# Optimization experiments

Hardware: AMD Instinct MI355X
Metric: run time of the kernel (lower is better)

## Reference

```python
import jax, jax.numpy as jnp
import numpy as np

MAXLEN = 20
NLAYERS = 4


def setup_inputs() -> dict:
    key = jax.random.key(0)
    ks = jax.random.split(key, 16)
    B, SRC, H, V = 256, 64, 1024, 32000
    s = 1.0 / np.sqrt(H)
    return {
        "encoder_outputs": jax.random.normal(ks[0], (B, SRC, H), jnp.float32),
        "encoder_hidden": jax.random.normal(ks[1], (NLAYERS, B, H), jnp.float32),
        "emb_table": jax.random.normal(ks[2], (V, H), jnp.float32) * s,
        "gru_w_ih": jax.random.normal(ks[3], (NLAYERS, 3 * H, H), jnp.float32) * s,
        "gru_w_hh": jax.random.normal(ks[4], (NLAYERS, 3 * H, H), jnp.float32) * s,
        "gru_b_ih": jax.random.normal(ks[5], (NLAYERS, 3 * H), jnp.float32) * s,
        "gru_b_hh": jax.random.normal(ks[6], (NLAYERS, 3 * H), jnp.float32) * s,
        "out_w": jax.random.normal(ks[7], (V, H), jnp.float32) * s,
        "out_b": jax.random.normal(ks[8], (V,), jnp.float32) * s,
        "l1_w": jax.random.normal(ks[9], (3, 2 * H), jnp.float32) * s,
        "l1_b": jax.random.normal(ks[10], (3,), jnp.float32) * s,
        "l2_w": jax.random.normal(ks[11], (1, 3), jnp.float32),
        "l2_b": jax.random.normal(ks[12], (1,), jnp.float32),
    }


def _gru_layer(x, h, w_ih, w_hh, b_ih, b_hh):
    # PyTorch GRU gate order: r, z, n
    gi = x @ w_ih.T + b_ih  # [B, 3H]
    gh = h @ w_hh.T + b_hh  # [B, 3H]
    i_r, i_z, i_n = jnp.split(gi, 3, axis=-1)
    h_r, h_z, h_n = jnp.split(gh, 3, axis=-1)
    r = jax.nn.sigmoid(i_r + h_r)
    z = jax.nn.sigmoid(i_z + h_z)
    n = jnp.tanh(i_n + r * h_n)
    return (1.0 - z) * n + z * h


def reference(encoder_outputs, encoder_hidden, emb_table, gru_w_ih, gru_w_hh,
              gru_b_ih, gru_b_hh, out_w, out_b, l1_w, l1_b, l2_w, l2_b):
    B = encoder_outputs.shape[0]
    enc_h0 = encoder_hidden[0]  # [B, H]

    def step(carry, _):
        h, tok = carry  # h: [4,B,H], tok: [B] int32
        # attention-score branch (computed in torch but unused -> DCE'd by jit)
        a = jnp.broadcast_to(h[0, -1], enc_h0.shape)
        enc = jnp.concatenate([a, enc_h0], axis=1)  # [B, 2H]
        _align = jax.nn.softmax((enc @ l1_w.T + l1_b) @ l2_w.T + l2_b, axis=0)
        # embedding + relu + 4-layer GRU (seq len 1)
        x = jax.nn.relu(emb_table[tok])  # [B, H]
        hs = []
        for l in range(NLAYERS):
            hl = _gru_layer(x, h[l], gru_w_ih[l], gru_w_hh[l], gru_b_ih[l], gru_b_hh[l])
            hs.append(hl)
            x = hl
        h = jnp.stack(hs)  # [4, B, H]
        logits = x @ out_w.T + out_b  # [B, V]
        tok = jnp.argmax(logits, axis=-1).astype(jnp.int32)  # greedy (topk(1))
        return (h, tok), logits

    tok0 = jnp.zeros((B,), jnp.int32)
    (h_final, _), logits = jax.lax.scan(step, (encoder_hidden, tok0), None, length=MAXLEN)
    # [T,B,V] -> [B,T,V], then log_softmax over vocab
    log_probs = jax.nn.log_softmax(jnp.transpose(logits, (1, 0, 2)), axis=-1)
    return log_probs, h_final
```

## Files before the change

### kernel.cpp

```cpp
#include <hip/hip_runtime.h>
#include <math.h>

#define HD 1024
#define NBATCH 256
#define VOC 32000
#define TSTEPS 20
#define OUT_ROW 640000LL
#define BH ((size_t)NBATCH * HD)
#define NCHUNK 500
#define THR 0.125f

typedef _Float16 f16;
typedef __attribute__((ext_vector_type(4))) _Float16 f16x4;
typedef __attribute__((ext_vector_type(8))) _Float16 f16x8;
typedef __attribute__((ext_vector_type(4))) float f32x4;

#define GLOBAL_AS __attribute__((address_space(1)))
#define LDS_AS    __attribute__((address_space(3)))

static __device__ __forceinline__ float sigmoidf_(float v) {
  return 1.0f / (1.0f + expf(-v));
}


__global__ void f32_to_f16_k(const float* __restrict__ in, f16* __restrict__ out, long n8) {
  long i = (long)blockIdx.x * 256 + threadIdx.x;
  long stride = (long)gridDim.x * 256;
  for (; i < n8; i += stride) {
    float4 a = *((const float4*)in + i * 2);
    float4 b = *((const float4*)in + i * 2 + 1);
    f16x8 o;
    o[0] = (f16)a.x; o[1] = (f16)a.y; o[2] = (f16)a.z; o[3] = (f16)a.w;
    o[4] = (f16)b.x; o[5] = (f16)b.y; o[6] = (f16)b.z; o[7] = (f16)b.w;
    *((f16x8*)out + i) = o;
  }
}

__global__ void split_f32_k(const float* __restrict__ in, f16* __restrict__ hi,
                            f16* __restrict__ lo, long n8) {
  long i = (long)blockIdx.x * 256 + threadIdx.x;
  long stride = (long)gridDim.x * 256;
  for (; i < n8; i += stride) {
    float4 a = *((const float4*)in + i * 2);
    float4 b = *((const float4*)in + i * 2 + 1);
    float v[8] = {a.x, a.y, a.z, a.w, b.x, b.y, b.z, b.w};
    f16x8 h8, l8;
    #pragma unroll
    for (int j = 0; j < 8; ++j) {
      f16 h = (f16)v[j];
      h8[j] = h;
      l8[j] = (f16)(v[j] - (float)h);
    }
    *((f16x8*)hi + i) = h8;
    *((f16x8*)lo + i) = l8;
  }
}

__global__ __launch_bounds__(256)
void gemm_gru_mfma4_k(const f16* __restrict__ a0_hi, const f16* __restrict__ a0_lo,
                      const f16* __restrict__ a1_hi, const f16* __restrict__ a1_lo,
                      const float* __restrict__ emb, const int* __restrict__ tok, int use_emb,
                      const float* __restrict__ w_ih, const float* __restrict__ w_hh,
                      float* __restrict__ gg2) {
  __shared__ f16x8 atoms[2][1088];

  const int tid = threadIdx.x;
  const int lane = tid & 63;
  const int wave = tid >> 6;
  const int wm = wave >> 1, wn = wave & 1;
  const int l15 = lane & 15, l4 = lane >> 4;
  const int n0g = blockIdx.x * 64;
  const int m0 = blockIdx.y * 64;
  const int kb = blockIdx.z * 512;

  const f16 *ahi, *alo; const float* W; int nc;
  if (n0g < 3072) { ahi = a0_hi; alo = a0_lo; W = w_ih; nc = n0g; }
  else            { ahi = a1_hi; alo = a1_lo; W = w_hh; nc = n0g - 3072; }
  const bool embmode = use_emb && (n0g < 3072);

  f32x4 acc[2][2];
  #pragma unroll
  for (int mi = 0; mi < 2; ++mi)
    #pragma unroll
    for (int ni = 0; ni < 2; ++ni) acc[mi][ni] = (f32x4){0.f, 0.f, 0.f, 0.f};

  const int sr = tid >> 2, skg = tid & 3;
  const int satom = skg * 68 + sr;
  const float* wgp = W + (size_t)(nc + sr) * HD + kb + skg * 8;
  const f16* agh = ahi + (size_t)(m0 + sr) * HD + kb + skg * 8;
  const f16* agl = alo + (size_t)(m0 + sr) * HD + kb + skg * 8;
  const float* egp = embmode ? (emb + (size_t)tok[m0 + sr] * HD + kb + skg * 8) : wgp;

  #define LOADREGS(k0, rah, ral, wbh, wbl) { \
    if (embmode) { \
      float4 e0 = *(const float4*)(egp + (k0)); \
      float4 e1 = *(const float4*)(egp + (k0) + 4); \
      float av[8] = {fmaxf(e0.x,0.f), fmaxf(e0.y,0.f), fmaxf(e0.z,0.f), fmaxf(e0.w,0.f), \
                     fmaxf(e1.x,0.f), fmaxf(e1.y,0.f), fmaxf(e1.z,0.f), fmaxf(e1.w,0.f)}; \
      _Pragma("unroll") \
      for (int j = 0; j < 8; ++j) { \
        f16 h = (f16)av[j]; rah[j] = h; ral[j] = (f16)(av[j] - (float)h); \
      } \
    } else { \
      rah = *(const f16x8*)(agh + (k0)); \
      ral = *(const f16x8*)(agl + (k0)); \
    } \
    float4 w0 = *(const float4*)(wgp + (k0)); \
    float4 w1 = *(const float4*)(wgp + (k0) + 4); \
    float wv[8] = {w0.x, w0.y, w0.z, w0.w, w1.x, w1.y, w1.z, w1.w}; \
    _Pragma("unroll") \
    for (int j = 0; j < 8; ++j) { \
      f16 h = (f16)wv[j]; wbh[j] = h; wbl[j] = (f16)(wv[j] - (float)h); \
    } }

  {
    f16x8 rah, ral, wbh, wbl;
    LOADREGS(0, rah, ral, wbh, wbl);
    atoms[0][satom]       = rah;
    atoms[0][272 + satom] = ral;
    atoms[0][544 + satom] = wbh;
    atoms[0][816 + satom] = wbl;
  }
  __syncthreads();

  for (int kt = 0; kt < 16; ++kt) {
    const int cur = kt & 1;
    f16x8 nah, nal, nbh, nbl;
    if (kt < 15) { LOADREGS((kt + 1) * 32, nah, nal, nbh, nbl); }

    f16x8 fah[2], fal[2], fbh[2], fbl[2];
    #pragma unroll
    for (int mi = 0; mi < 2; ++mi) {
      int idx = l4 * 68 + wm * 32 + mi * 16 + l15;
      fah[mi] = atoms[cur][idx];
      fal[mi] = atoms[cur][272 + idx];
    }
    #pragma unroll
    for (int ni = 0; ni < 2; ++ni) {
      int idx = l4 * 68 + wn * 32 + ni * 16 + l15;
      fbh[ni] = atoms[cur][544 + idx];
      fbl[ni] = atoms[cur][816 + idx];
    }
    #pragma unroll
    for (int mi = 0; mi < 2; ++mi)
      #pragma unroll
      for (int ni = 0; ni < 2; ++ni) {
        acc[mi][ni] = __builtin_amdgcn_mfma_f32_16x16x32_f16(fah[mi], fbh[ni], acc[mi][ni], 0, 0, 0);
        acc[mi][ni] = __builtin_amdgcn_mfma_f32_16x16x32_f16(fah[mi], fbl[ni], acc[mi][ni], 0, 0, 0);
        acc[mi][ni] = __builtin_amdgcn_mfma_f32_16x16x32_f16(fal[mi], fbh[ni], acc[mi][ni], 0, 0, 0);
      }

    if (kt < 15) {
      atoms[cur ^ 1][satom]       = nah;
      atoms[cur ^ 1][272 + satom] = nal;
      atoms[cur ^ 1][544 + satom] = nbh;
      atoms[cur ^ 1][816 + satom] = nbl;
    }
    __syncthreads();
  }
  #undef LOADREGS

  float* outp = gg2 + (size_t)blockIdx.z * NBATCH * 6144;
  #pragma unroll
  for (int mi = 0; mi < 2; ++mi)
    #pragma unroll
    for (int ni = 0; ni < 2; ++ni) {
      const int col = n0g + wn * 32 + ni * 16 + l15;
      #pragma unroll
      for (int r = 0; r < 4; ++r) {
        const int row = m0 + wm * 32 + mi * 16 + l4 * 4 + r;
        outp[(size_t)row * 6144 + col] = acc[mi][ni][r];
      }
    }
}

static __device__ __forceinline__ float4 add4_(float4 a, float4 b) {
  float4 r; r.x = a.x + b.x; r.y = a.y + b.y; r.z = a.z + b.z; r.w = a.w + b.w; return r;
}
__global__ void gru_gates_split2_k(const float* __restrict__ gg2,
                                   const float* __restrict__ b_ih, const float* __restrict__ b_hh,
                                   const f16* __restrict__ hold_hi, const f16* __restrict__ hold_lo,
                                   f16* __restrict__ hnew_hi, f16* __restrict__ hnew_lo) {
  int idx = blockIdx.x * 256 + threadIdx.x;
  int b = idx >> 8;
  int k4 = (idx & 255) << 2;
  const float* g0 = gg2 + (size_t)b * 6144;
  const float* g1 = gg2 + (size_t)NBATCH * 6144 + (size_t)b * 6144;
  #define LD2(off) add4_(*(const float4*)(g0 + (off) + k4), *(const float4*)(g1 + (off) + k4))
  float4 gir = LD2(0);
  float4 giz = LD2(1024);
  float4 gin = LD2(2048);
  float4 ghr = LD2(3072);
  float4 ghz = LD2(4096);
  float4 ghn = LD2(5120);
  #undef LD2
  float4 bir = *(const float4*)(b_ih + k4);
  float4 biz = *(const float4*)(b_ih + 1024 + k4);
  float4 bin = *(const float4*)(b_ih + 2048 + k4);
  float4 bhr = *(const float4*)(b_hh + k4);
  float4 bhz = *(const float4*)(b_hh + 1024 + k4);
  float4 bhn = *(const float4*)(b_hh + 2048 + k4);
  f16x4 hh = *(const f16x4*)(hold_hi + (size_t)b * HD + k4);
  f16x4 hl = *(const f16x4*)(hold_lo + (size_t)b * HD + k4);
  float hov[4];
  #pragma unroll
  for (int j = 0; j < 4; ++j) hov[j] = (float)hh[j] + (float)hl[j];
  float4 ho; ho.x = hov[0]; ho.y = hov[1]; ho.z = hov[2]; ho.w = hov[3];
  float4 o;
  #define GATE(c) { \
    float rr = sigmoidf_(gir.c + bir.c + ghr.c + bhr.c); \
    float zz = sigmoidf_(giz.c + biz.c + ghz.c + bhz.c); \
    float nn = tanhf(gin.c + bin.c + rr * (ghn.c + bhn.c)); \
    o.c = (1.0f - zz) * nn + zz * ho.c; }
  GATE(x) GATE(y) GATE(z) GATE(w)
  #undef GATE
  float vv[4] = {o.x, o.y, o.z, o.w};
  f16x4 h4, l4;
  #pragma unroll
  for (int j = 0; j < 4; ++j) {
    f16 h = (f16)vv[j];
    h4[j] = h;
    l4[j] = (f16)(vv[j] - (float)h);
  }
  *(f16x4*)(hnew_hi + (size_t)b * HD + k4) = h4;
  *(f16x4*)(hnew_lo + (size_t)b * HD + k4) = l4;
}

__global__ __launch_bounds__(256)
void gemm_logits3_k(const f16* __restrict__ xf, const f16* __restrict__ wf,
                    const float* __restrict__ bias, float* __restrict__ scr,
                    float* __restrict__ pmax, float* __restrict__ psum) {
  __shared__ f16 lb[2][2112];
  const int tid = threadIdx.x;
  const int lane = tid & 63;
  const int wave = tid >> 6;
  const int l15 = lane & 15, l4 = lane >> 4;
  const int chunk = blockIdx.x;
  const int n0 = chunk * 64;

  f32x4 acc[4][4];
  #pragma unroll
  for (int mi = 0; mi < 4; ++mi)
    #pragma unroll
    for (int ni = 0; ni < 4; ++ni) acc[mi][ni] = (f32x4){0.f, 0.f, 0.f, 0.f};

  f16x8 a_cur[4], a_nxt[4];

  #define STAGE(k0, buf) { \
    const f16* src = wf + (size_t)(n0 + lane) * 1024 + (k0) + wave * 8; \
    __builtin_amdgcn_global_load_lds((const GLOBAL_AS void*)src, \
        (LDS_AS void*)(lb[buf] + wave * 528), 16, 0, 0); }
  #define LOADA(k0, dst) { \
    _Pragma("unroll") \
    for (int mi = 0; mi < 4; ++mi) { \
      int row = wave * 64 + mi * 16 + l15; \
      dst[mi] = *(const f16x8*)(xf + (size_t)row * 1024 + (k0) + l4 * 8); \
    } }

  STAGE(0, 0);
  LOADA(0, a_cur);
  __syncthreads();

  for (int kt = 0; kt < 32; ++kt) {
    const int cur = kt & 1;
    f16x8 b[4];
    #pragma unroll
    for (int ni = 0; ni < 4; ++ni)
      b[ni] = *(const f16x8*)(lb[cur] + (size_t)l4 * 528 + (size_t)(ni * 16 + l15) * 8);
    if (kt < 31) {
      STAGE((kt + 1) * 32, cur ^ 1);
      LOADA((kt + 1) * 32, a_nxt);
    }
    #pragma unroll
    for (int mi = 0; mi < 4; ++mi)
      #pragma unroll
      for (int ni = 0; ni < 4; ++ni)
        acc[mi][ni] = __builtin_amdgcn_mfma_f32_16x16x32_f16(a_cur[mi], b[ni], acc[mi][ni], 0, 0, 0);
    __syncthreads();
    #pragma unroll
    for (int mi = 0; mi < 4; ++mi) a_cur[mi] = a_nxt[mi];
  }
  #undef STAGE
  #undef LOADA

  float bv[4];
  #pragma unroll
  for (int ni = 0; ni < 4; ++ni) bv[ni] = bias[n0 + ni * 16 + l15];

  #pragma unroll
  for (int mi = 0; mi < 4; ++mi) {
    #pragma unroll
    for (int r = 0; r < 4; ++r) {
      const int row = wave * 64 + mi * 16 + l4 * 4 + r;
      float v[4];
      #pragma unroll
      for (int ni = 0; ni < 4; ++ni) {
        v[ni] = acc[mi][ni][r] + bv[ni];
        scr[(size_t)row * VOC + n0 + ni * 16 + l15] = v[ni];
      }
      float m = fmaxf(fmaxf(v[0], v[1]), fmaxf(v[2], v[3]));
      #pragma unroll
      for (int d = 1; d < 16; d <<= 1) m = fmaxf(m, __shfl_xor(m, d, 64));
      float s = __expf(v[0] - m) + __expf(v[1] - m) + __expf(v[2] - m) + __expf(v[3] - m);
      #pragma unroll
      for (int d = 1; d < 16; d <<= 1) s += __shfl_xor(s, d, 64);
      if (l15 == 0) {
        pmax[(size_t)row * NCHUNK + chunk] = m;
        psum[(size_t)row * NCHUNK + chunk] = s;
      }
    }
  }
}

__global__ __launch_bounds__(256)
void token_k(const float* __restrict__ pmax, const float* __restrict__ psum,
             const float* __restrict__ lg,
             const f16* __restrict__ xhi, const f16* __restrict__ xlo,
             const float* __restrict__ w, const float* __restrict__ ob,
             float* __restrict__ lse_out, int* __restrict__ tok) {
  __shared__ float sm[256];
  __shared__ float ssum[256];
  __shared__ double sd[256];
  __shared__ int sfl[16];
  __shared__ int scand[32];
  __shared__ int sflc, scnt;
  const int b = blockIdx.x;
  const int tid = threadIdx.x;
  const float* PM = pmax + (size_t)b * NCHUNK;
  const float* PS = psum + (size_t)b * NCHUNK;

  float m = -3.4e38f, s = 0.0f;
  for (int c = tid; c < NCHUNK; c += 256) {
    float mc = PM[c], sc = PS[c];
    float M = fmaxf(m, mc);
    s = s * __expf(m - M) + sc * __expf(mc - M);
    m = M;
  }
  sm[tid] = m; ssum[tid] = s;
  if (tid == 0) { sflc = 0; scnt = 0; }
  __syncthreads();
  for (int off = 128; off; off >>= 1) {
    if (tid < off) {
      float m1 = sm[tid], m2 = sm[tid + off];
      float M = fmaxf(m1, m2);
      ssum[tid] = ssum[tid] * __expf(m1 - M) + ssum[tid + off] * __expf(m2 - M);
      sm[tid] = M;
    }
    __syncthreads();
  }
  const float gmax = sm[0];
  const float lse = gmax + logf(ssum[0]);
  if (tid == 0) lse_out[b] = lse;
  const float thr = gmax - THR;

  for (int c = tid; c < NCHUNK; c += 256) {
    if (PM[c] >= thr) {
      int p = atomicAdd(&sflc, 1);
      if (p < 16) sfl[p] = c;
    }
  }
  __syncthreads();
  const int nf = sflc < 16 ? sflc : 16;

  const int g = tid >> 6, li = tid & 63;
  for (int f0 = 0; f0 < nf; f0 += 4) {
    int f = f0 + g;
    if (f < nf) {
      float v = lg[(size_t)b * VOC + sfl[f] * 64 + li];
      if (v >= thr) {
        int p = atomicAdd(&scnt, 1);
        if (p < 32) scand[p] = sfl[f] * 64 + li;
      }
    }
  }
  __syncthreads();
  const int c = scnt < 32 ? scnt : 32;

  if (c == 1) {
    if (tid == 0) tok[b] = scand[0];
    return;
  }

  double best = -1.0e300; int bi = 0x7fffffff;
  for (int j = 0; j < c; ++j) {
    const int idx = scand[j];
    double p = 0.0;
    const f16* xh = xhi + (size_t)b * HD;
    const f16* xl = xlo + (size_t)b * HD;
    const float* wr = w + (size_t)idx * HD;
    for (int k = tid; k < HD; k += 256)
      p += ((double)xh[k] + (double)xl[k]) * (double)wr[k];
    sd[tid] = p;
    __syncthreads();
    for (int off = 128; off; off >>= 1) {
      if (tid < off) sd[tid] += sd[tid + off];
      __syncthreads();
    }
    if (tid == 0) sd[0] += (double)ob[idx];
    __syncthreads();
    double tot = sd[0];
    if (tot > best || (tot == best && idx < bi)) { best = tot; bi = idx; }
    __syncthreads();
  }
  if (tid == 0) tok[b] = bi;
}

__global__ void write_out_k(const float* __restrict__ scr, const float* __restrict__ lse,
                            float* __restrict__ outp) {
  int idx = blockIdx.x * 256 + threadIdx.x;
  int b = idx / 8000;
  int r = idx - b * 8000;
  float l = lse[b];
  float4 v = ((const float4*)(scr + (size_t)b * VOC))[r];
  v.x -= l; v.y -= l; v.z -= l; v.w -= l;
  ((float4*)(outp + (size_t)b * OUT_ROW))[r] = v;
}

__global__ void combine_h_k(const f16* __restrict__ hi, const f16* __restrict__ lo,
                            float* __restrict__ o, int n4) {
  int i = blockIdx.x * 256 + threadIdx.x;
  if (i >= n4) return;
  f16x4 h = ((const f16x4*)hi)[i];
  f16x4 l = ((const f16x4*)lo)[i];
  float4 v;
  v.x = (float)h[0] + (float)l[0];
  v.y = (float)h[1] + (float)l[1];
  v.z = (float)h[2] + (float)l[2];
  v.w = (float)h[3] + (float)l[3];
  ((float4*)o)[i] = v;
}

extern "C" void kernel_launch(void* const* d_in, const int* in_sizes, int n_in,
                              void* d_out, int out_size, void* d_ws, size_t ws_size,
                              hipStream_t stream) {
  (void)in_sizes; (void)n_in; (void)out_size;
  const float* enc_hidden = (const float*)d_in[1];
  const float* emb   = (const float*)d_in[2];
  const float* w_ih  = (const float*)d_in[3];
  const float* w_hh  = (const float*)d_in[4];
  const float* b_ih  = (const float*)d_in[5];
  const float* b_hh  = (const float*)d_in[6];
  const float* out_w = (const float*)d_in[7];
  const float* out_b = (const float*)d_in[8];
  float* out = (float*)d_out;

  size_t off = 0;
  char* base = (char*)d_ws;
  #define WSALLOC(bytes) ((void*)(base + off)); off += (((size_t)(bytes)) + 255) & ~(size_t)255
  float* gg2     = (float*) WSALLOC((size_t)2 * NBATCH * 6144 * 4);
  f16*   hs_hi   = (f16*)   WSALLOC(2 * 4 * BH * 2);
  f16*   hs_lo   = (f16*)   WSALLOC(2 * 4 * BH * 2);
  int*   tok     = (int*)   WSALLOC(1024);
  float* pmax    = (float*) WSALLOC((size_t)NBATCH * NCHUNK * 4);
  float* psum    = (float*) WSALLOC((size_t)NBATCH * NCHUNK * 4);
  float* lse_all = (float*) WSALLOC((size_t)TSTEPS * NBATCH * 4);
  f16*   wf16    = (f16*)   WSALLOC((size_t)VOC * HD * 2);
  float* lgws    = (float*) WSALLOC((size_t)NBATCH * VOC * 4);
  #undef WSALLOC
  if (off > ws_size) return;

  f32_to_f16_k<<<2048, 256, 0, stream>>>(out_w, wf16, (long)VOC * HD / 8);
  split_f32_k<<<512, 256, 0, stream>>>(enc_hidden, hs_hi, hs_lo, (long)(4 * BH / 8));
  hipMemsetAsync(tok, 0, NBATCH * 4, stream);

  int p = 0;
  for (int t = 0; t < TSTEPS; ++t) {
    f16* hp_hi = hs_hi + (size_t)p * 4 * BH;
    f16* hp_lo = hs_lo + (size_t)p * 4 * BH;
    f16* hn_hi = hs_hi + (size_t)(1 - p) * 4 * BH;
    f16* hn_lo = hs_lo + (size_t)(1 - p) * 4 * BH;

    for (int l = 0; l < 4; ++l) {
      const f16* a0hi = (l == 0) ? hs_hi : hn_hi + (size_t)(l - 1) * BH;
      const f16* a0lo = (l == 0) ? hs_lo : hn_lo + (size_t)(l - 1) * BH;
      gemm_gru_mfma4_k<<<dim3(96, 4, 2), 256, 0, stream>>>(
          a0hi, a0lo, hp_hi + (size_t)l * BH, hp_lo + (size_t)l * BH,
          emb, tok, (l == 0) ? 1 : 0,
          w_ih + (size_t)l * 3072 * HD, w_hh + (size_t)l * 3072 * HD, gg2);
      gru_gates_split2_k<<<256, 256, 0, stream>>>(
          gg2, b_ih + l * 3072, b_hh + l * 3072,
          hp_hi + (size_t)l * BH, hp_lo + (size_t)l * BH,
          hn_hi + (size_t)l * BH, hn_lo + (size_t)l * BH);
    }

    gemm_logits3_k<<<NCHUNK, 256, 0, stream>>>(
        hn_hi + (size_t)3 * BH, wf16, out_b, lgws, pmax, psum);
    token_k<<<NBATCH, 256, 0, stream>>>(
        pmax, psum, lgws, hn_hi + (size_t)3 * BH, hn_lo + (size_t)3 * BH,
        out_w, out_b, lse_all + (size_t)t * NBATCH, tok);
    write_out_k<<<8000, 256, 0, stream>>>(
        lgws, lse_all + (size_t)t * NBATCH, out + (size_t)t * VOC);

    p ^= 1;
  }

  combine_h_k<<<1024, 256, 0, stream>>>(hs_hi, hs_lo,
                                        out + (size_t)NBATCH * TSTEPS * VOC,
                                        (int)(4 * BH / 4));
}
```

Measured before the change: 4.068 ms.

## Pre-split GRU weights to f16 hi/lo and stream them via global_load_lds

The GRU weights are split once per call into f16 hi/lo arrays, so the per-step GEMM no longer converts fp32 weights inside its inner loop. The weight tiles are copied into LDS with direct global-to-LDS loads. The A operand (activations or embeddings) is now loaded straight into registers in MFMA fragment layout, so it skips LDS. This removes the repeated conversion work across 20 timesteps and cuts LDS traffic, at the cost of extra workspace and a one-time split pass over about 100 MB of weights. The A loads are less coalesced (16-byte loads spread across rows).

```diff
diff --git a/kernel.cpp b/kernel.cpp
--- a/kernel.cpp
+++ b/kernel.cpp
@@ -57,12 +57,14 @@
 }
 
 __global__ __launch_bounds__(256)
-void gemm_gru_mfma4_k(const f16* __restrict__ a0_hi, const f16* __restrict__ a0_lo,
+void gemm_gru_mfma7_k(const f16* __restrict__ a0_hi, const f16* __restrict__ a0_lo,
                       const f16* __restrict__ a1_hi, const f16* __restrict__ a1_lo,
                       const float* __restrict__ emb, const int* __restrict__ tok, int use_emb,
-                      const float* __restrict__ w_ih, const float* __restrict__ w_hh,
+                      const f16* __restrict__ wih_hi, const f16* __restrict__ wih_lo,
+                      const f16* __restrict__ whh_hi, const f16* __restrict__ whh_lo,
                       float* __restrict__ gg2) {
-  __shared__ f16x8 atoms[2][1088];
+  __shared__ f16 lbh[2][2112];
+  __shared__ f16 lbl[2][2112];
 
   const int tid = threadIdx.x;
   const int lane = tid & 63;
@@ -73,9 +75,9 @@
   const int m0 = blockIdx.y * 64;
   const int kb = blockIdx.z * 512;
 
-  const f16 *ahi, *alo; const float* W; int nc;
-  if (n0g < 3072) { ahi = a0_hi; alo = a0_lo; W = w_ih; nc = n0g; }
-  else            { ahi = a1_hi; alo = a1_lo; W = w_hh; nc = n0g - 3072; }
+  const f16 *ahi, *alo, *whi, *wlo; int nc;
+  if (n0g < 3072) { ahi = a0_hi; alo = a0_lo; whi = wih_hi; wlo = wih_lo; nc = n0g; }
+  else            { ahi = a1_hi; alo = a1_lo; whi = whh_hi; wlo = whh_lo; nc = n0g - 3072; }
   const bool embmode = use_emb && (n0g < 3072);
 
   f32x4 acc[2][2];
@@ -84,81 +86,74 @@
     #pragma unroll
     for (int ni = 0; ni < 2; ++ni) acc[mi][ni] = (f32x4){0.f, 0.f, 0.f, 0.f};
 
-  const int sr = tid >> 2, skg = tid & 3;
-  const int satom = skg * 68 + sr;
-  const float* wgp = W + (size_t)(nc + sr) * HD + kb + skg * 8;
-  const f16* agh = ahi + (size_t)(m0 + sr) * HD + kb + skg * 8;
-  const f16* agl = alo + (size_t)(m0 + sr) * HD + kb + skg * 8;
-  const float* egp = embmode ? (emb + (size_t)tok[m0 + sr] * HD + kb + skg * 8) : wgp;
-
-  #define LOADREGS(k0, rah, ral, wbh, wbl) { \
+  const int arow0 = m0 + wm * 32 + l15;
+  const f16* ap_h = ahi + (size_t)arow0 * HD + kb + l4 * 8;
+  const f16* ap_l = alo + (size_t)arow0 * HD + kb + l4 * 8;
+  const float* ep0 = embmode ? (emb + (size_t)tok[arow0] * HD + kb + l4 * 8) : (const float*)0;
+  const float* ep1 = embmode ? (emb + (size_t)tok[arow0 + 16] * HD + kb + l4 * 8) : (const float*)0;
+
+  #define STAGE(kt, buf) { \
+    const size_t so = (size_t)(nc + lane) * HD + kb + (kt) * 32 + wave * 8; \
+    __builtin_amdgcn_global_load_lds((const GLOBAL_AS void*)(whi + so), \
+        (LDS_AS void*)(lbh[buf] + wave * 528), 16, 0, 0); \
+    __builtin_amdgcn_global_load_lds((const GLOBAL_AS void*)(wlo + so), \
+        (LDS_AS void*)(lbl[buf] + wave * 528), 16, 0, 0); }
+
+  #define LOADA(kt, dh, dl) { \
     if (embmode) { \
-      float4 e0 = *(const float4*)(egp + (k0)); \
-      float4 e1 = *(const float4*)(egp + (k0) + 4); \
-      float av[8] = {fmaxf(e0.x,0.f), fmaxf(e0.y,0.f), fmaxf(e0.z,0.f), fmaxf(e0.w,0.f), \
-                     fmaxf(e1.x,0.f), fmaxf(e1.y,0.f), fmaxf(e1.z,0.f), fmaxf(e1.w,0.f)}; \
       _Pragma("unroll") \
-      for (int j = 0; j < 8; ++j) { \
-        f16 h = (f16)av[j]; rah[j] = h; ral[j] = (f16)(av[j] - (float)h); \
+      for (int mi = 0; mi < 2; ++mi) { \
+        const float* ep = mi ? ep1 : ep0; \
+        float4 e0 = *(const float4*)(ep + (kt) * 32); \
+        float4 e1 = *(const float4*)(ep + (kt) * 32 + 4); \
+        float av[8] = {fmaxf(e0.x,0.f), fmaxf(e0.y,0.f), fmaxf(e0.z,0.f), fmaxf(e0.w,0.f), \
+                       fmaxf(e1.x,0.f), fmaxf(e1.y,0.f), fmaxf(e1.z,0.f), fmaxf(e1.w,0.f)}; \
+        _Pragma("unroll") \
+        for (int j = 0; j < 8; ++j) { \
+          f16 h = (f16)av[j]; dh[mi][j] = h; dl[mi][j] = (f16)(av[j] - (float)h); \
+        } \
       } \
     } else { \
-      rah = *(const f16x8*)(agh + (k0)); \
-      ral = *(const f16x8*)(agl + (k0)); \
-    } \
-    float4 w0 = *(const float4*)(wgp + (k0)); \
-    float4 w1 = *(const float4*)(wgp + (k0) + 4); \
-    float wv[8] = {w0.x, w0.y, w0.z, w0.w, w1.x, w1.y, w1.z, w1.w}; \
-    _Pragma("unroll") \
-    for (int j = 0; j < 8; ++j) { \
-      f16 h = (f16)wv[j]; wbh[j] = h; wbl[j] = (f16)(wv[j] - (float)h); \
+      dh[0] = *(const f16x8*)(ap_h + (kt) * 32); \
+      dh[1] = *(const f16x8*)(ap_h + (size_t)16 * HD + (kt) * 32); \
+      dl[0] = *(const f16x8*)(ap_l + (kt) * 32); \
+      dl[1] = *(const f16x8*)(ap_l + (size_t)16 * HD + (kt) * 32); \
     } }
 
-  {
-    f16x8 rah, ral, wbh, wbl;
-    LOADREGS(0, rah, ral, wbh, wbl);
-    atoms[0][satom]       = rah;
-    atoms[0][272 + satom] = ral;
-    atoms[0][544 + satom] = wbh;
-    atoms[0][816 + satom] = wbl;
-  }
+  f16x8 ach[2], acl[2], anh[2], anl[2];
+  STAGE(0, 0);
+  LOADA(0, ach, acl);
   __syncthreads();
 
   for (int kt = 0; kt < 16; ++kt) {
     const int cur = kt & 1;
-    f16x8 nah, nal, nbh, nbl;
-    if (kt < 15) { LOADREGS((kt + 1) * 32, nah, nal, nbh, nbl); }
-
-    f16x8 fah[2], fal[2], fbh[2], fbl[2];
-    #pragma unroll
-    for (int mi = 0; mi < 2; ++mi) {
-      int idx = l4 * 68 + wm * 32 + mi * 16 + l15;
-      fah[mi] = atoms[cur][idx];
-      fal[mi] = atoms[cur][272 + idx];
-    }
+    f16x8 fbh[2], fbl[2];
     #pragma unroll
     for (int ni = 0; ni < 2; ++ni) {
-      int idx = l4 * 68 + wn * 32 + ni * 16 + l15;
-      fbh[ni] = atoms[cur][544 + idx];
-      fbl[ni] = atoms[cur][816 + idx];
+      const int off = l4 * 528 + (wn * 32 + ni * 16 + l15) * 8;
+      fbh[ni] = *(const f16x8*)(lbh[cur] + off);
+      fbl[ni] = *(const f16x8*)(lbl[cur] + off);
+    }
+    if (kt < 15) {
+      STAGE(kt + 1, cur ^ 1);
+      LOADA(kt + 1, anh, anl);
     }
     #pragma unroll
     for (int mi = 0; mi < 2; ++mi)
       #pragma unroll
       for (int ni = 0; ni < 2; ++ni) {
-        acc[mi][ni] = __builtin_amdgcn_mfma_f32_16x16x32_f16(fah[mi], fbh[ni], acc[mi][ni], 0, 0, 0);
-        acc[mi][ni] = __builtin_amdgcn_mfma_f32_16x16x32_f16(fah[mi], fbl[ni], acc[mi][ni], 0, 0, 0);
-        acc[mi][ni] = __builtin_amdgcn_mfma_f32_16x16x32_f16(fal[mi], fbh[ni], acc[mi][ni], 0, 0, 0);
+        acc[mi][ni] = __builtin_amdgcn_mfma_f32_16x16x32_f16(ach[mi], fbh[ni], acc[mi][ni], 0, 0, 0);
+        acc[mi][ni] = __builtin_amdgcn_mfma_f32_16x16x32_f16(ach[mi], fbl[ni], acc[mi][ni], 0, 0, 0);
+        acc[mi][ni] = __builtin_amdgcn_mfma_f32_16x16x32_f16(acl[mi], fbh[ni], acc[mi][ni], 0, 0, 0);
       }
-
+    __syncthreads();
     if (kt < 15) {
-      atoms[cur ^ 1][satom]       = nah;
-      atoms[cur ^ 1][272 + satom] = nal;
-      atoms[cur ^ 1][544 + satom] = nbh;
-      atoms[cur ^ 1][816 + satom] = nbl;
-    }
-    __syncthreads();
-  }
-  #undef LOADREGS
+      #pragma unroll
+      for (int mi = 0; mi < 2; ++mi) { ach[mi] = anh[mi]; acl[mi] = anl[mi]; }
+    }
+  }
+  #undef STAGE
+  #undef LOADA
 
   float* outp = gg2 + (size_t)blockIdx.z * NBATCH * 6144;
   #pragma unroll
@@ -456,10 +451,16 @@
   float* lse_all = (float*) WSALLOC((size_t)TSTEPS * NBATCH * 4);
   f16*   wf16    = (f16*)   WSALLOC((size_t)VOC * HD * 2);
   float* lgws    = (float*) WSALLOC((size_t)NBATCH * VOC * 4);
+  f16*   wih_hi  = (f16*)   WSALLOC((size_t)4 * 3072 * HD * 2);
+  f16*   wih_lo  = (f16*)   WSALLOC((size_t)4 * 3072 * HD * 2);
+  f16*   whh_hi  = (f16*)   WSALLOC((size_t)4 * 3072 * HD * 2);
+  f16*   whh_lo  = (f16*)   WSALLOC((size_t)4 * 3072 * HD * 2);
   #undef WSALLOC
   if (off > ws_size) return;
 
   f32_to_f16_k<<<2048, 256, 0, stream>>>(out_w, wf16, (long)VOC * HD / 8);
+  split_f32_k<<<2048, 256, 0, stream>>>(w_ih, wih_hi, wih_lo, (long)4 * 3072 * HD / 8);
+  split_f32_k<<<2048, 256, 0, stream>>>(w_hh, whh_hi, whh_lo, (long)4 * 3072 * HD / 8);
   split_f32_k<<<512, 256, 0, stream>>>(enc_hidden, hs_hi, hs_lo, (long)(4 * BH / 8));
   hipMemsetAsync(tok, 0, NBATCH * 4, stream);
 
@@ -473,10 +474,11 @@
     for (int l = 0; l < 4; ++l) {
       const f16* a0hi = (l == 0) ? hs_hi : hn_hi + (size_t)(l - 1) * BH;
       const f16* a0lo = (l == 0) ? hs_lo : hn_lo + (size_t)(l - 1) * BH;
-      gemm_gru_mfma4_k<<<dim3(96, 4, 2), 256, 0, stream>>>(
+      gemm_gru_mfma7_k<<<dim3(96, 4, 2), 256, 0, stream>>>(
           a0hi, a0lo, hp_hi + (size_t)l * BH, hp_lo + (size_t)l * BH,
           emb, tok, (l == 0) ? 1 : 0,
-          w_ih + (size_t)l * 3072 * HD, w_hh + (size_t)l * 3072 * HD, gg2);
+          wih_hi + (size_t)l * 3072 * HD, wih_lo + (size_t)l * 3072 * HD,
+          whh_hi + (size_t)l * 3072 * HD, whh_lo + (size_t)l * 3072 * HD, gg2);
       gru_gates_split2_k<<<256, 256, 0, stream>>>(
           gg2, b_ih + l * 3072, b_hh + l * 3072,
           hp_hi + (size_t)l * BH, hp_lo + (size_t)l * BH,
```

After: 5.628 ms. +38.3%, slower.
